# Performance work log

Measured on AMD Instinct MI355X. Metric: run time of the kernel, lower is better.

Reference implementation:

```python
import jax, jax.numpy as jnp
import numpy as np

N, M, K, D = 8192, 64, 256, 16  # n_vecs, subvector_num, ksub (2**subvector_bits), dsub


def setup_inputs() -> dict:
    key = jax.random.key(0)
    k1, k2 = jax.random.split(key)
    vecs = jax.random.normal(k1, (N, M * D), dtype=jnp.float32)
    codebook = jax.random.normal(k2, (M, K, D), dtype=jnp.float32)
    return {"vecs": vecs, "codebook": codebook}


def reference(vecs, codebook):
    # quantization pipeline: code_selection -> get_index -> quantized_vecs
    n = vecs.shape[0]
    m, k, d = codebook.shape
    v = vecs.reshape(n, m, d)
    # proba = -||v - c||^2 computed via expansion (same math, no [N,M,K,D] broadcast)
    v2 = jnp.sum(v * v, axis=-1)[:, :, None]            # [N,M,1]
    c2 = jnp.sum(codebook * codebook, axis=-1)[None]    # [1,M,K]
    vc = jnp.einsum('nmd,mkd->nmk', v, codebook)        # [N,M,K]
    proba = -(v2 - 2.0 * vc + c2)
    # softmax is monotonic -> argmax(softmax(proba)) == argmax(proba)
    index = jnp.argmax(proba, axis=-1)                  # [N,M] int
    # quantized_vecs: one-hot scatter + matmul == gather of selected codewords
    quantized = codebook[jnp.arange(m)[None, :], index] # [N,M,D]
    return quantized.reshape(n, m * d)
```

## Files before the change

kernel.cpp:

```cpp
#include <hip/hip_runtime.h>
#include <math.h>

#define M_SUB 64
#define K_CODES 256
#define D_DIM 16
#define ROW_F 1024
#define THRGAP 0.0078125f
#define TILE_B 1088
#define SLICE_B (16 * TILE_B)

typedef __attribute__((ext_vector_type(8))) short short8;
typedef __attribute__((ext_vector_type(4))) float f32x4;

__device__ inline unsigned bfr(float x) {
    unsigned u = __builtin_bit_cast(unsigned, x);
    return (u + 0x7FFFu + ((u >> 16) & 1u)) >> 16;
}
__device__ inline float bff(unsigned h) { return __builtin_bit_cast(float, h << 16); }

template <int C> __device__ inline float dppf(float x) {
    return __builtin_bit_cast(float,
        __builtin_amdgcn_update_dpp(0, __builtin_bit_cast(int, x), C, 0xF, 0xF, true));
}
template <int C> __device__ inline int dppi(int x) {
    return __builtin_amdgcn_update_dpp(0, x, C, 0xF, 0xF, true);
}

__global__ __launch_bounds__(256) void pq_convert_kernel(
    const float* __restrict__ cb, char* __restrict__ pk)
{
    const int m = blockIdx.x, k = threadIdx.x;
    const float* cp = cb + ((size_t)m * K_CODES + k) * D_DIM;
    float f[16];
    #pragma unroll
    for (int q = 0; q < 4; ++q) {
        float4 t4 = ((const float4*)cp)[q];
        f[q*4+0] = t4.x; f[q*4+1] = t4.y; f[q*4+2] = t4.z; f[q*4+3] = t4.w;
    }
    float c2 = 0.f;
    #pragma unroll
    for (int d = 0; d < 16; ++d) c2 = fmaf(f[d], f[d], c2);
    short hi[16], lo[16];
    #pragma unroll
    for (int d = 0; d < 16; ++d) {
        unsigned h = bfr(f[d]);
        hi[d] = (short)h;
        lo[d] = (short)bfr(f[d] - bff(h));
    }
    char* tb = pk + (size_t)m * SLICE_B + (k >> 4) * TILE_B;
    const int lr = k & 15;
    short8 v0 = { hi[0],hi[1],hi[2],hi[3],hi[4],hi[5],hi[6],hi[7] };
    short8 v1 = { hi[8],hi[9],hi[10],hi[11],hi[12],hi[13],hi[14],hi[15] };
    short8 v2 = { lo[0],lo[1],lo[2],lo[3],lo[4],lo[5],lo[6],lo[7] };
    short8 v3 = { lo[8],lo[9],lo[10],lo[11],lo[12],lo[13],lo[14],lo[15] };
    *(short8*)(tb +   0 + lr * 16) = v0;
    *(short8*)(tb + 256 + lr * 16) = v1;
    *(short8*)(tb + 512 + lr * 16) = v2;
    *(short8*)(tb + 768 + lr * 16) = v3;
    *(float*)(tb + 1024 + lr * 4) = -c2;
}

__global__ __launch_bounds__(256, 2) void pq_mfma_kernel(
    const float* __restrict__ vecs, const float* __restrict__ cb,
    float* __restrict__ out, const char* __restrict__ pk)
{
    const int tid  = threadIdx.x;
    const int w    = tid >> 6;
    const int lane = tid & 63;
    const int lr   = lane & 15;
    const int lg   = lane >> 4;
    const int wid  = blockIdx.x * 4 + w;
    const int m    = wid >> 8;
    const int n0   = (wid & 255) * 32;

    __shared__ unsigned IDXW[4][8];
    __shared__ unsigned FLGW[4][8];

    const char* pkm = pk + (size_t)m * SLICE_B;

    float nc2v[16];
    #pragma unroll
    for (int kt = 0; kt < 16; ++kt)
        nc2v[kt] = *(const float*)(pkm + kt * TILE_B + 1024 + lr * 4);

    short8 A1[2], A2[2];
    #pragma unroll
    for (int t = 0; t < 2; ++t) {
        const float* vp = vecs + (size_t)(n0 + t * 16 + lr) * ROW_F + m * D_DIM + (lg & 1) * 8;
        float4 a4 = ((const float4*)vp)[0];
        float4 b4 = ((const float4*)vp)[1];
        float f[8];
        f[0]=2.f*a4.x; f[1]=2.f*a4.y; f[2]=2.f*a4.z; f[3]=2.f*a4.w;
        f[4]=2.f*b4.x; f[5]=2.f*b4.y; f[6]=2.f*b4.z; f[7]=2.f*b4.w;
        short hi[8], lo[8];
        #pragma unroll
        for (int e = 0; e < 8; ++e) {
            unsigned h = bfr(f[e]);
            hi[e] = (short)h;
            lo[e] = (short)bfr(f[e] - bff(h));
        }
        short8 H = { hi[0],hi[1],hi[2],hi[3],hi[4],hi[5],hi[6],hi[7] };
        short8 L = { lo[0],lo[1],lo[2],lo[3],lo[4],lo[5],lo[6],lo[7] };
        const bool hiSide = (lg < 2);
        A1[t] = hiSide ? H : L;
        A2[t] = hiSide ? L : H;
    }

    f32x4 acc[2][16];
    #pragma unroll
    for (int kt = 0; kt < 16; ++kt) {
        short8 B = *(const short8*)(pkm + kt * TILE_B + lane * 16);
        float nv = nc2v[kt];
        f32x4 c0 = { nv, nv, nv, nv };
        f32x4 c1 = { nv, nv, nv, nv };
        c0 = __builtin_amdgcn_mfma_f32_16x16x32_bf16(A1[0], B, c0, 0, 0, 0);
        c0 = __builtin_amdgcn_mfma_f32_16x16x32_bf16(A2[0], B, c0, 0, 0, 0);
        c1 = __builtin_amdgcn_mfma_f32_16x16x32_bf16(A1[1], B, c1, 0, 0, 0);
        c1 = __builtin_amdgcn_mfma_f32_16x16x32_bf16(A2[1], B, c1, 0, 0, 0);
        acc[0][kt] = c0;
        acc[1][kt] = c1;
    }

    #pragma unroll
    for (int t = 0; t < 2; ++t) {
        unsigned kp[4]; unsigned rf = 0;
        #pragma unroll
        for (int p = 0; p < 4; ++p) {
            float x0 = fmaxf(fmaxf(acc[t][0][p],  acc[t][1][p]),  acc[t][2][p]);
            float x1 = fmaxf(fmaxf(acc[t][3][p],  acc[t][4][p]),  acc[t][5][p]);
            float x2 = fmaxf(fmaxf(acc[t][6][p],  acc[t][7][p]),  acc[t][8][p]);
            float x3 = fmaxf(fmaxf(acc[t][9][p],  acc[t][10][p]), acc[t][11][p]);
            float x4 = fmaxf(fmaxf(acc[t][12][p], acc[t][13][p]), acc[t][14][p]);
            float b  = fmaxf(fmaxf(fmaxf(x0, x1), x2), fmaxf(fmaxf(x3, x4), acc[t][15][p]));
            b = fmaxf(b, dppf<0xB1>(b));
            b = fmaxf(b, dppf<0x4E>(b));
            b = fmaxf(b, dppf<0x141>(b));
            b = fmaxf(b, dppf<0x140>(b));
            const float bthr = b - THRGAP;
            unsigned Mm = 0;
            #pragma unroll
            for (int kt = 15; kt >= 0; --kt)
                Mm = Mm + Mm + (acc[t][kt][p] >= bthr ? 1u : 0u);
            int cl  = __popc(Mm);
            int bkt = __ffs(Mm) - 1;
            int bkv = Mm ? (bkt * 16 + lr) : 0x7FFFFFFF;
            cl += dppi<0xB1>(cl);  bkv = min(bkv, dppi<0xB1>(bkv));
            cl += dppi<0x4E>(cl);  bkv = min(bkv, dppi<0x4E>(bkv));
            cl += dppi<0x141>(cl); bkv = min(bkv, dppi<0x141>(bkv));
            cl += dppi<0x140>(cl); bkv = min(bkv, dppi<0x140>(bkv));
            if (bkv > 255) bkv = 0;
            kp[p] = (unsigned)bkv;
            rf |= (cl != 1) ? (1u << p) : 0u;
        }
        if (lr == 0) {
            IDXW[w][t * 4 + lg] = kp[0] | (kp[1] << 8) | (kp[2] << 16) | (kp[3] << 24);
            FLGW[w][t * 4 + lg] = rf;
        }
    }

    #pragma unroll 1
    for (int e = 0; e < 8; ++e) {
        unsigned rf = FLGW[w][e];
        if (rf) {
            #pragma unroll 1
            for (int p = 0; p < 4; ++p) if (rf & (1u << p)) {
                const int r = (e >> 2) * 16 + (e & 3) * 4 + p;
                const int n = n0 + r;
                const float* vrow = vecs + (size_t)n * ROW_F + m * D_DIM;
                double vd[16];
                #pragma unroll
                for (int d = 0; d < 16; ++d) vd[d] = (double)vrow[d];
                double bs = -1e300; int bi = 0;
                #pragma unroll
                for (int j = 0; j < 4; ++j) {
                    int k = lane * 4 + j;
                    const float* cp = cb + ((size_t)m * K_CODES + k) * D_DIM;
                    double vc = 0.0, c2 = 0.0;
                    #pragma unroll
                    for (int d = 0; d < 16; ++d) {
                        double cd = (double)cp[d];
                        vc = fma(vd[d], cd, vc);
                        c2 = fma(cd, cd, c2);
                    }
                    double s = 2.0 * vc - c2;
                    if (s > bs) { bs = s; bi = k; }
                }
                #pragma unroll
                for (int off = 32; off; off >>= 1) {
                    double so = __shfl_xor(bs, off, 64);
                    int    ko = __shfl_xor(bi, off, 64);
                    if (so > bs || (so == bs && ko < bi)) { bs = so; bi = ko; }
                }
                if (lane == 0) ((char*)&IDXW[w][e])[p] = (char)bi;
            }
        }
    }

    #pragma unroll
    for (int s = 0; s < 2; ++s) {
        const int r = s * 16 + (lane >> 2);
        unsigned e4 = IDXW[w][r >> 2];
        const int k = (int)((e4 >> ((r & 3) * 8)) & 255u);
        const float4* src = (const float4*)(cb + ((size_t)m * K_CODES + k) * D_DIM);
        float4 val = src[lane & 3];
        float4* dst = (float4*)(out + (size_t)(n0 + r) * ROW_F + m * D_DIM);
        dst[lane & 3] = val;
    }
}

extern "C" void kernel_launch(void* const* d_in, const int* in_sizes, int n_in,
                              void* d_out, int out_size, void* d_ws, size_t ws_size,
                              hipStream_t stream) {
    const float* vecs = (const float*)d_in[0];
    const float* cb   = (const float*)d_in[1];
    float* out        = (float*)d_out;
    char* pk          = (char*)d_ws;

    pq_convert_kernel<<<M_SUB, 256, 0, stream>>>(cb, pk);
    pq_mfma_kernel<<<4096, 256, 0, stream>>>(vecs, cb, out, pk);
}
```

Before: 60.09 us.

## Track running top-2 scores instead of storing all accumulators; raise occupancy

Replaces the 128-float accumulator array with a streaming per-lane best, second-best and best-index update after each MFMA tile. The cross-lane reduction now merges (best, second, index) triples, and the fallback flag fires when the gap between best and second is within the threshold. The lower register demand allows launch bounds to request 4 blocks per CU instead of 2. In exchange there are extra compares and selects inside the MFMA loop, which can serialise behind the MFMA results. Tie handling also changes slightly: the lowest index is no longer chosen among near-ties, though such rows still go to the exact fallback path.

New measurement: 68.78 us. +14.5%, slower.

```diff
diff --git a/kernel.cpp b/kernel.cpp
--- a/kernel.cpp
+++ b/kernel.cpp
@@ -24,6 +24,12 @@
 }
 template <int C> __device__ inline int dppi(int x) {
     return __builtin_amdgcn_update_dpp(0, x, C, 0xF, 0xF, true);
+}
+template <int C> __device__ inline void merge3(float& b, float& b2, int& bk) {
+    float bo = dppf<C>(b), b2o = dppf<C>(b2);
+    int   ko = dppi<C>(bk);
+    b2 = fmaxf(fmaxf(b2, b2o), fminf(b, bo));
+    if (bo > b) { b = bo; bk = ko; }
 }
 
 __global__ __launch_bounds__(256) void pq_convert_kernel(
@@ -60,7 +66,7 @@
     *(float*)(tb + 1024 + lr * 4) = -c2;
 }
 
-__global__ __launch_bounds__(256, 2) void pq_mfma_kernel(
+__global__ __launch_bounds__(256, 4) void pq_mfma_kernel(
     const float* __restrict__ vecs, const float* __restrict__ cb,
     float* __restrict__ out, const char* __restrict__ pk)
 {
@@ -106,7 +112,13 @@
         A2[t] = hiSide ? L : H;
     }
 
-    f32x4 acc[2][16];
+    float rb[2][4], rb2[2][4];
+    int   rbk[2][4];
+    #pragma unroll
+    for (int t = 0; t < 2; ++t)
+        #pragma unroll
+        for (int p = 0; p < 4; ++p) { rb[t][p] = -INFINITY; rb2[t][p] = -INFINITY; rbk[t][p] = 0; }
+
     #pragma unroll
     for (int kt = 0; kt < 16; ++kt) {
         short8 B = *(const short8*)(pkm + kt * TILE_B + lane * 16);
@@ -117,8 +129,16 @@
         c0 = __builtin_amdgcn_mfma_f32_16x16x32_bf16(A2[0], B, c0, 0, 0, 0);
         c1 = __builtin_amdgcn_mfma_f32_16x16x32_bf16(A1[1], B, c1, 0, 0, 0);
         c1 = __builtin_amdgcn_mfma_f32_16x16x32_bf16(A2[1], B, c1, 0, 0, 0);
-        acc[0][kt] = c0;
-        acc[1][kt] = c1;
+        const int kk = kt * 16 + lr;
+        #pragma unroll
+        for (int p = 0; p < 4; ++p) {
+            float v0 = c0[p];
+            rb2[0][p] = fmaxf(rb2[0][p], fminf(v0, rb[0][p]));
+            if (v0 > rb[0][p]) { rb[0][p] = v0; rbk[0][p] = kk; }
+            float v1 = c1[p];
+            rb2[1][p] = fmaxf(rb2[1][p], fminf(v1, rb[1][p]));
+            if (v1 > rb[1][p]) { rb[1][p] = v1; rbk[1][p] = kk; }
+        }
     }
 
     #pragma unroll
@@ -126,31 +146,14 @@
         unsigned kp[4]; unsigned rf = 0;
         #pragma unroll
         for (int p = 0; p < 4; ++p) {
-            float x0 = fmaxf(fmaxf(acc[t][0][p],  acc[t][1][p]),  acc[t][2][p]);
-            float x1 = fmaxf(fmaxf(acc[t][3][p],  acc[t][4][p]),  acc[t][5][p]);
-            float x2 = fmaxf(fmaxf(acc[t][6][p],  acc[t][7][p]),  acc[t][8][p]);
-            float x3 = fmaxf(fmaxf(acc[t][9][p],  acc[t][10][p]), acc[t][11][p]);
-            float x4 = fmaxf(fmaxf(acc[t][12][p], acc[t][13][p]), acc[t][14][p]);
-            float b  = fmaxf(fmaxf(fmaxf(x0, x1), x2), fmaxf(fmaxf(x3, x4), acc[t][15][p]));
-            b = fmaxf(b, dppf<0xB1>(b));
-            b = fmaxf(b, dppf<0x4E>(b));
-            b = fmaxf(b, dppf<0x141>(b));
-            b = fmaxf(b, dppf<0x140>(b));
-            const float bthr = b - THRGAP;
-            unsigned Mm = 0;
-            #pragma unroll
-            for (int kt = 15; kt >= 0; --kt)
-                Mm = Mm + Mm + (acc[t][kt][p] >= bthr ? 1u : 0u);
-            int cl  = __popc(Mm);
-            int bkt = __ffs(Mm) - 1;
-            int bkv = Mm ? (bkt * 16 + lr) : 0x7FFFFFFF;
-            cl += dppi<0xB1>(cl);  bkv = min(bkv, dppi<0xB1>(bkv));
-            cl += dppi<0x4E>(cl);  bkv = min(bkv, dppi<0x4E>(bkv));
-            cl += dppi<0x141>(cl); bkv = min(bkv, dppi<0x141>(bkv));
-            cl += dppi<0x140>(cl); bkv = min(bkv, dppi<0x140>(bkv));
-            if (bkv > 255) bkv = 0;
-            kp[p] = (unsigned)bkv;
-            rf |= (cl != 1) ? (1u << p) : 0u;
+            float b = rb[t][p], b2 = rb2[t][p];
+            int bk = rbk[t][p];
+            merge3<0xB1>(b, b2, bk);
+            merge3<0x4E>(b, b2, bk);
+            merge3<0x141>(b, b2, bk);
+            merge3<0x140>(b, b2, bk);
+            kp[p] = (unsigned)bk & 255u;
+            rf |= (!(b - b2 > THRGAP)) ? (1u << p) : 0u;
         }
         if (lr == 0) {
             IDXW[w][t * 4 + lg] = kp[0] | (kp[1] << 8) | (kp[2] << 16) | (kp[3] << 24);
```

## Process 64 rows per wave in a rolled loop, raising occupancy target

Applied to the files above, without the earlier changes.

Each wave now handles 64 rows (four 16-row tiles) instead of 32, and loops over the tiles one at a time with a non-unrolled loop, so only 16 accumulators stay live instead of 32. Launch bounds are raised to 4 blocks per CU and the grid is halved. The codebook slice pointer is forced into scalar registers via readfirstlane so B loads use scalar addressing. The cost is re-reading B tiles for every row tile and giving up the MFMA interleave across two tiles, in exchange for lower register pressure and more resident waves.

After: 103.9 us. +72.8%, slower.

```diff
diff --git a/kernel.cpp b/kernel.cpp
--- a/kernel.cpp
+++ b/kernel.cpp
@@ -60,7 +60,7 @@
     *(float*)(tb + 1024 + lr * 4) = -c2;
 }
 
-__global__ __launch_bounds__(256, 2) void pq_mfma_kernel(
+__global__ __launch_bounds__(256, 4) void pq_mfma_kernel(
     const float* __restrict__ vecs, const float* __restrict__ cb,
     float* __restrict__ out, const char* __restrict__ pk)
 {
@@ -70,22 +70,30 @@
     const int lr   = lane & 15;
     const int lg   = lane >> 4;
     const int wid  = blockIdx.x * 4 + w;
-    const int m    = wid >> 8;
-    const int n0   = (wid & 255) * 32;
-
-    __shared__ unsigned IDXW[4][8];
-    __shared__ unsigned FLGW[4][8];
-
-    const char* pkm = pk + (size_t)m * SLICE_B;
+    const int m    = wid >> 7;
+    const int n0   = (wid & 127) * 64;
+
+    __shared__ unsigned IDXW[4][16];
+    __shared__ unsigned FLGW[4][16];
+
+    const char* pkm_v = pk + (size_t)m * SLICE_B;
+    unsigned long long upv = (unsigned long long)pkm_v;
+    unsigned plo = __builtin_amdgcn_readfirstlane((unsigned)upv);
+    unsigned phi = __builtin_amdgcn_readfirstlane((unsigned)(upv >> 32));
+    unsigned long long up0 = ((unsigned long long)phi << 32) | plo;
+    const char* pkm = (const char*)up0;
 
     float nc2v[16];
     #pragma unroll
     for (int kt = 0; kt < 16; ++kt)
         nc2v[kt] = *(const float*)(pkm + kt * TILE_B + 1024 + lr * 4);
 
-    short8 A1[2], A2[2];
-    #pragma unroll
-    for (int t = 0; t < 2; ++t) {
+    #pragma unroll 1
+    for (int t = 0; t < 4; ++t) {
+        unsigned long long up = up0;
+        asm volatile("" : "+s"(up));
+        const char* pkt = (const char*)up;
+
         const float* vp = vecs + (size_t)(n0 + t * 16 + lr) * ROW_F + m * D_DIM + (lg & 1) * 8;
         float4 a4 = ((const float4*)vp)[0];
         float4 b4 = ((const float4*)vp)[1];
@@ -102,36 +110,29 @@
         short8 H = { hi[0],hi[1],hi[2],hi[3],hi[4],hi[5],hi[6],hi[7] };
         short8 L = { lo[0],lo[1],lo[2],lo[3],lo[4],lo[5],lo[6],lo[7] };
         const bool hiSide = (lg < 2);
-        A1[t] = hiSide ? H : L;
-        A2[t] = hiSide ? L : H;
-    }
-
-    f32x4 acc[2][16];
-    #pragma unroll
-    for (int kt = 0; kt < 16; ++kt) {
-        short8 B = *(const short8*)(pkm + kt * TILE_B + lane * 16);
-        float nv = nc2v[kt];
-        f32x4 c0 = { nv, nv, nv, nv };
-        f32x4 c1 = { nv, nv, nv, nv };
-        c0 = __builtin_amdgcn_mfma_f32_16x16x32_bf16(A1[0], B, c0, 0, 0, 0);
-        c0 = __builtin_amdgcn_mfma_f32_16x16x32_bf16(A2[0], B, c0, 0, 0, 0);
-        c1 = __builtin_amdgcn_mfma_f32_16x16x32_bf16(A1[1], B, c1, 0, 0, 0);
-        c1 = __builtin_amdgcn_mfma_f32_16x16x32_bf16(A2[1], B, c1, 0, 0, 0);
-        acc[0][kt] = c0;
-        acc[1][kt] = c1;
-    }
-
-    #pragma unroll
-    for (int t = 0; t < 2; ++t) {
+        short8 A1 = hiSide ? H : L;
+        short8 A2 = hiSide ? L : H;
+
+        f32x4 acc[16];
+        #pragma unroll
+        for (int kt = 0; kt < 16; ++kt) {
+            short8 B = *(const short8*)(pkt + kt * TILE_B + lane * 16);
+            float nv = nc2v[kt];
+            f32x4 c0 = { nv, nv, nv, nv };
+            c0 = __builtin_amdgcn_mfma_f32_16x16x32_bf16(A1, B, c0, 0, 0, 0);
+            c0 = __builtin_amdgcn_mfma_f32_16x16x32_bf16(A2, B, c0, 0, 0, 0);
+            acc[kt] = c0;
+        }
+
         unsigned kp[4]; unsigned rf = 0;
         #pragma unroll
         for (int p = 0; p < 4; ++p) {
-            float x0 = fmaxf(fmaxf(acc[t][0][p],  acc[t][1][p]),  acc[t][2][p]);
-            float x1 = fmaxf(fmaxf(acc[t][3][p],  acc[t][4][p]),  acc[t][5][p]);
-            float x2 = fmaxf(fmaxf(acc[t][6][p],  acc[t][7][p]),  acc[t][8][p]);
-            float x3 = fmaxf(fmaxf(acc[t][9][p],  acc[t][10][p]), acc[t][11][p]);
-            float x4 = fmaxf(fmaxf(acc[t][12][p], acc[t][13][p]), acc[t][14][p]);
-            float b  = fmaxf(fmaxf(fmaxf(x0, x1), x2), fmaxf(fmaxf(x3, x4), acc[t][15][p]));
+            float x0 = fmaxf(fmaxf(acc[0][p],  acc[1][p]),  acc[2][p]);
+            float x1 = fmaxf(fmaxf(acc[3][p],  acc[4][p]),  acc[5][p]);
+            float x2 = fmaxf(fmaxf(acc[6][p],  acc[7][p]),  acc[8][p]);
+            float x3 = fmaxf(fmaxf(acc[9][p],  acc[10][p]), acc[11][p]);
+            float x4 = fmaxf(fmaxf(acc[12][p], acc[13][p]), acc[14][p]);
+            float b  = fmaxf(fmaxf(fmaxf(x0, x1), x2), fmaxf(fmaxf(x3, x4), acc[15][p]));
             b = fmaxf(b, dppf<0xB1>(b));
             b = fmaxf(b, dppf<0x4E>(b));
             b = fmaxf(b, dppf<0x141>(b));
@@ -140,7 +141,7 @@
             unsigned Mm = 0;
             #pragma unroll
             for (int kt = 15; kt >= 0; --kt)
-                Mm = Mm + Mm + (acc[t][kt][p] >= bthr ? 1u : 0u);
+                Mm = Mm + Mm + (acc[kt][p] >= bthr ? 1u : 0u);
             int cl  = __popc(Mm);
             int bkt = __ffs(Mm) - 1;
             int bkv = Mm ? (bkt * 16 + lr) : 0x7FFFFFFF;
@@ -159,7 +160,7 @@
     }
 
     #pragma unroll 1
-    for (int e = 0; e < 8; ++e) {
+    for (int e = 0; e < 16; ++e) {
         unsigned rf = FLGW[w][e];
         if (rf) {
             #pragma unroll 1
@@ -197,7 +198,7 @@
     }
 
     #pragma unroll
-    for (int s = 0; s < 2; ++s) {
+    for (int s = 0; s < 4; ++s) {
         const int r = s * 16 + (lane >> 2);
         unsigned e4 = IDXW[w][r >> 2];
         const int k = (int)((e4 >> ((r & 3) * 8)) & 255u);
@@ -217,5 +218,5 @@
     char* pk          = (char*)d_ws;
 
     pq_convert_kernel<<<M_SUB, 256, 0, stream>>>(cb, pk);
-    pq_mfma_kernel<<<4096, 256, 0, stream>>>(vecs, cb, out, pk);
-}
+    pq_mfma_kernel<<<2048, 256, 0, stream>>>(vecs, cb, out, pk);
+}
```
